# Kernel tuning notes

Measured on AMD Instinct MI355X. Metric: run time of the kernel, lower is better.

## Reference

```python
import jax, jax.numpy as jnp
from jax import lax
import numpy as np

B, C_IN, F, T = 8, 16, 1024, 512
D = 1024          # rnn_hidden_size == rnn_input_size
L = 4             # rnn_num_layers
N_TOKENS = 512
RES_REDUCE = 2


def setup_inputs() -> dict:
    key = jax.random.key(0)
    ks = jax.random.split(key, 8)
    fused_feats = jax.random.normal(ks[0], (B, C_IN, F, T), dtype=jnp.float32)
    s_audio_length = jax.random.randint(ks[1], (B,), 1, T + 1, dtype=jnp.int64)
    # 1x1 conv: C_IN -> 1 channel
    conv_w = jax.random.normal(ks[2], (C_IN,), dtype=jnp.float32) * (1.0 / np.sqrt(C_IN))
    conv_b = jnp.zeros((1,), dtype=jnp.float32)
    # SRU per-layer params (all layers have d_in == D): W [L, D, 3D], v [L, 2D], b [L, 2D]
    sru_W = jax.random.normal(ks[3], (L, D, 3 * D), dtype=jnp.float32) * (1.0 / np.sqrt(D))
    sru_v = jax.random.normal(ks[4], (L, 2 * D), dtype=jnp.float32) * 0.1
    sru_b = jnp.zeros((L, 2 * D), dtype=jnp.float32)
    fc_w = jax.random.normal(ks[5], (D, N_TOKENS), dtype=jnp.float32) * (1.0 / np.sqrt(D))
    fc_b = jnp.zeros((N_TOKENS,), dtype=jnp.float32)
    return dict(fused_feats=fused_feats, s_audio_length=s_audio_length,
                conv_w=conv_w, conv_b=conv_b,
                sru_W=sru_W, sru_v=sru_v, sru_b=sru_b,
                fc_w=fc_w, fc_b=fc_b)


def _sru_layer(x, W, v, b):
    # x: [T, B, D]; W: [D, 3D]; v, b: [2D]
    d = W.shape[1] // 3
    U = jnp.einsum('tbi,ik->tbk', x, W).reshape(x.shape[0], x.shape[1], 3, d)
    x_tilde, f_pre, r_pre = U[..., 0, :], U[..., 1, :], U[..., 2, :]
    vf, vr = v[:d], v[d:]
    bf, br = b[:d], b[d:]

    def step(c, inp):
        xt_t, fp_t = inp
        f = jax.nn.sigmoid(fp_t + vf * c + bf)
        c_new = f * c + (1.0 - f) * xt_t
        return c_new, c_new

    c0 = jnp.zeros((x.shape[1], d), dtype=x.dtype)
    _, cs = lax.scan(step, c0, (x_tilde, f_pre))            # cs: [T, B, D]
    r = jax.nn.sigmoid(r_pre + vr * cs + br)                # reset uses c_t
    return r * cs + (1.0 - r) * x                           # highway residual


def reference(fused_feats, s_audio_length, conv_w, conv_b, sru_W, sru_v, sru_b, fc_w, fc_b):
    # 1x1 conv over channel dim + ReLU: [B, C, F, T] -> [B, F, T]
    x = jax.nn.relu(jnp.einsum('bcft,c->bft', fused_feats, conv_w) + conv_b[0])
    x = x.transpose(2, 0, 1)                                # [T, B, F]
    for l in range(L):
        x = _sru_layer(x, sru_W[l], sru_v[l], sru_b[l])
    rnn_out = x.transpose(1, 0, 2)                          # [B, T, D]
    tokens_logits = jnp.einsum('btd,dk->btk', rnn_out, fc_w) + fc_b
    return tokens_logits, s_audio_length // RES_REDUCE
```

## Files before the change

kernel.cpp:

```cpp
#include <hip/hip_runtime.h>
#include <cstddef>
#include <cstdint>

static constexpr int B_  = 8;
static constexpr int CIN = 16;
static constexpr int F_  = 1024;
static constexpr int T_  = 512;
static constexpr int D_  = 1024;
static constexpr int L_  = 4;
static constexpr int NT  = 512;
static constexpr int M_  = T_ * B_;
static constexpr int K3  = 3 * D_;
static constexpr int NP  = 4 * D_;

typedef __attribute__((ext_vector_type(8))) short short8;
typedef __attribute__((ext_vector_type(4))) float floatx4;

__device__ __forceinline__ unsigned short f2bf(float f) {
    unsigned int u = __builtin_bit_cast(unsigned int, f);
    u += 0x7FFFu + ((u >> 16) & 1u);
    return (unsigned short)(u >> 16);
}
__device__ __forceinline__ float bf2f(unsigned short s) {
    unsigned int u = ((unsigned int)s) << 16;
    return __builtin_bit_cast(float, u);
}

#define GLD16(g, l)                                                              \
    __builtin_amdgcn_global_load_lds(                                            \
        (__attribute__((address_space(1))) unsigned int*)(g),                    \
        (__attribute__((address_space(3))) unsigned int*)(l), 16, 0, 0)

__global__ __launch_bounds__(256) void conv_relu_tr(
    const float* __restrict__ feats, const float* __restrict__ wv,
    const float* __restrict__ bv, unsigned short* __restrict__ x0) {
    __shared__ float tile[32][68];
    const int b  = blockIdx.z;
    const int f0 = blockIdx.y * 32;
    const int t0 = blockIdx.x * 64;
    const float bias = bv[0];

    const int t4 = threadIdx.x & 15;
    const int fi = threadIdx.x >> 4;
    #pragma unroll
    for (int fo = 0; fo < 32; fo += 16) {
        const int f = fo + fi;
        float4 acc = {bias, bias, bias, bias};
        const float* p = feats + (((size_t)b * CIN) * F_ + (f0 + f)) * T_ + t0 + t4 * 4;
        #pragma unroll
        for (int c = 0; c < CIN; ++c) {
            const float4 vv = *(const float4*)(p + (size_t)c * F_ * T_);
            const float w = wv[c];
            acc.x += w * vv.x; acc.y += w * vv.y;
            acc.z += w * vv.z; acc.w += w * vv.w;
        }
        acc.x = fmaxf(acc.x, 0.f); acc.y = fmaxf(acc.y, 0.f);
        acc.z = fmaxf(acc.z, 0.f); acc.w = fmaxf(acc.w, 0.f);
        *(float4*)&tile[f][t4 * 4] = acc;
    }
    __syncthreads();
    const int f4 = threadIdx.x & 7;
    const int tr = threadIdx.x >> 3;
    #pragma unroll
    for (int to = 0; to < 64; to += 32) {
        const int t = to + tr;
        unsigned short pk[4];
        #pragma unroll
        for (int q = 0; q < 4; ++q) pk[q] = f2bf(tile[f4 * 4 + q][t]);
        *(uint2*)&x0[(size_t)(t0 + t) * (B_ * D_) + (size_t)b * D_ + f0 + f4 * 4] =
            *(const uint2*)pk;
    }
}

__global__ __launch_bounds__(256) void prep_weights(
    const float* __restrict__ sru_W, const float* __restrict__ fc_w,
    unsigned short* __restrict__ Wt, unsigned short* __restrict__ WtF) {
    __shared__ float tile[32][33];
    const int z  = blockIdx.z;
    const int x  = threadIdx.x & 31;
    const int y8 = threadIdx.x >> 5;
    if (z < 16) {
        const int l = z >> 2, j = z & 3;
        const int d0 = blockIdx.x * 32;
        const int k0 = blockIdx.y * 32;
        unsigned short* Wo = Wt + (size_t)l * ((size_t)NP * D_);
        if (j < 3) {
            const float* W = sru_W + (size_t)l * D_ * K3;
            #pragma unroll
            for (int yo = 0; yo < 32; yo += 8)
                tile[yo + y8][x] = W[(size_t)(k0 + yo + y8) * K3 + j * D_ + d0 + x];
            __syncthreads();
            #pragma unroll
            for (int yo = 0; yo < 32; yo += 8) {
                const int dy = yo + y8;
                Wo[(size_t)((d0 + dy) * 4 + j) * D_ + k0 + x] = f2bf(tile[x][dy]);
            }
        } else {
            #pragma unroll
            for (int yo = 0; yo < 32; yo += 8) {
                const int dy = d0 + yo + y8;
                Wo[(size_t)(dy * 4 + 3) * D_ + k0 + x] =
                    (k0 + x == dy) ? (unsigned short)0x3F80u : (unsigned short)0u;
            }
        }
    } else {
        if (blockIdx.x >= NT / 32) return;
        const int n0 = blockIdx.x * 32;
        const int k0 = blockIdx.y * 32;
        #pragma unroll
        for (int yo = 0; yo < 32; yo += 8)
            tile[yo + y8][x] = fc_w[(size_t)(k0 + yo + y8) * NT + n0 + x];
        __syncthreads();
        #pragma unroll
        for (int yo = 0; yo < 32; yo += 8)
            WtF[(size_t)(n0 + yo + y8) * D_ + k0 + x] = f2bf(tile[x][yo + y8]);
    }
}

template <int MODE>
__global__ __launch_bounds__(256) void gemm_mfma(
    const unsigned short* __restrict__ A,
    const unsigned short* __restrict__ Bt,
    void* __restrict__ Cv, const float* __restrict__ bias,
    int N, int K) {
    __shared__ unsigned short As[128 * 32];
    __shared__ unsigned short Bs[128 * 32];

    const int tid  = threadIdx.x;
    const int lane = tid & 63;
    const int wid  = tid >> 6;
    const int m0 = blockIdx.y * 128;
    const int n0 = blockIdx.x * 128;
    const int wm = (wid >> 1) * 64;
    const int wn = (wid & 1) * 64;

    floatx4 acc[4][4];
    #pragma unroll
    for (int mi = 0; mi < 4; ++mi)
        #pragma unroll
        for (int ni = 0; ni < 4; ++ni)
            acc[mi][ni] = (floatx4){0.f, 0.f, 0.f, 0.f};

    const char* gA = (const char*)A;
    const char* gB = (const char*)Bt;
    const size_t rowstride = (size_t)K * 2;
    const size_t rA0 = (size_t)(m0 + (tid >> 2)) * rowstride + (tid & 3) * 16;
    const size_t rB0 = (size_t)(n0 + (tid >> 2)) * rowstride + (tid & 3) * 16;
    const size_t pstep = 64 * rowstride;
    char* sA = (char*)As;
    char* sB = (char*)Bs;
    const int ldsbase = wid * 1024;

    const int rsel = lane & 15;
    const int koff = (lane >> 4) * 16;

    for (int k0 = 0; k0 < K; k0 += 32) {
        const size_t kb = (size_t)k0 * 2;
        GLD16(gA + rA0 + kb,         sA + ldsbase);
        GLD16(gA + rA0 + kb + pstep, sA + ldsbase + 4096);
        GLD16(gB + rB0 + kb,         sB + ldsbase);
        GLD16(gB + rB0 + kb + pstep, sB + ldsbase + 4096);
        __syncthreads();

        short8 af[4], bfv[4];
        #pragma unroll
        for (int mi = 0; mi < 4; ++mi)
            af[mi] = *(const short8*)(sA + ((wm + mi * 16 + rsel) * 64 + koff));
        #pragma unroll
        for (int ni = 0; ni < 4; ++ni)
            bfv[ni] = *(const short8*)(sB + ((wn + ni * 16 + rsel) * 64 + koff));
        #pragma unroll
        for (int mi = 0; mi < 4; ++mi)
            #pragma unroll
            for (int ni = 0; ni < 4; ++ni)
                acc[mi][ni] = __builtin_amdgcn_mfma_f32_16x16x32_bf16(
                    af[mi], bfv[ni], acc[mi][ni], 0, 0, 0);
        __syncthreads();
    }

    const int cl = lane & 15;
    const int qr = lane >> 4;
    #pragma unroll
    for (int mi = 0; mi < 4; ++mi) {
        #pragma unroll
        for (int ni = 0; ni < 4; ++ni) {
            const int gn = n0 + wn + ni * 16 + cl;
            #pragma unroll
            for (int i = 0; i < 4; ++i) {
                const int gm = m0 + wm + mi * 16 + qr * 4 + i;
                if (MODE == 0) {
                    ((unsigned short*)Cv)[(size_t)gm * N + gn] = f2bf(acc[mi][ni][i]);
                } else {
                    const int t  = gm >> 3;
                    const int bb = gm & 7;
                    ((float*)Cv)[((size_t)bb * T_ + t) * NT + gn] =
                        acc[mi][ni][i] + bias[gn];
                }
            }
        }
    }
}

__global__ __launch_bounds__(64) void sru_scan(
    const unsigned short* __restrict__ U4,
    const float* __restrict__ v, const float* __restrict__ bvec,
    unsigned short* __restrict__ h) {
    const int idx = blockIdx.x * 64 + threadIdx.x;
    const int d  = idx & (D_ - 1);

    const float vfn = -v[d];
    const float vrn = -v[D_ + d];
    const float bf_ = bvec[d];
    const float br_ = bvec[D_ + d];

    const uint2* up = (const uint2*)U4 + idx;
    unsigned short* hp = h + idx;

    constexpr int UNR  = 8;
    constexpr int PIPE = 4;
    constexpr int NB   = T_ / UNR;
    constexpr size_t ST = (size_t)B_ * D_;

    uint2 ub[PIPE][UNR];
    #pragma unroll
    for (int p = 0; p < PIPE; ++p)
        #pragma unroll
        for (int j = 0; j < UNR; ++j)
            ub[p][j] = up[(size_t)(p * UNR + j) * ST];

    float c = 0.0f;
    for (int bt = 0; bt < NB; bt += PIPE) {
        #pragma unroll
        for (int p = 0; p < PIPE; ++p) {
            const int s = bt + p;
            #pragma unroll
            for (int j = 0; j < UNR; ++j) {
                const uint2 u = ub[p][j];
                const float xt  = bf2f((unsigned short)(u.x & 0xFFFFu));
                const float fpp = bf2f((unsigned short)(u.x >> 16));
                const float rpp = bf2f((unsigned short)(u.y & 0xFFFFu));
                const float xi  = bf2f((unsigned short)(u.y >> 16));
                const float e1 = __expf(fmaf(vfn, c, -(fpp + bf_)));
                const float f  = __builtin_amdgcn_rcpf(1.0f + e1);
                c = fmaf(f, c - xt, xt);
                const float e2 = __expf(fmaf(vrn, c, -(rpp + br_)));
                const float r  = __builtin_amdgcn_rcpf(1.0f + e2);
                hp[(size_t)(s * UNR + j) * ST] = f2bf(fmaf(r, c - xi, xi));
            }
            if (s + PIPE < NB) {
                #pragma unroll
                for (int j = 0; j < UNR; ++j)
                    ub[p][j] = up[(size_t)((s + PIPE) * UNR + j) * ST];
            }
        }
    }
}

__global__ void lens_k(const int* __restrict__ lens, float* __restrict__ out) {
    const int i = threadIdx.x;
    if (i < B_) out[i] = (float)(lens[i] >> 1);
}

extern "C" void kernel_launch(void* const* d_in, const int* in_sizes, int n_in,
                              void* d_out, int out_size, void* d_ws, size_t ws_size,
                              hipStream_t stream) {
    const float* feats  = (const float*)d_in[0];
    const int*   lens   = (const int*)d_in[1];
    const float* conv_w = (const float*)d_in[2];
    const float* conv_b = (const float*)d_in[3];
    const float* sru_W  = (const float*)d_in[4];
    const float* sru_v  = (const float*)d_in[5];
    const float* sru_b  = (const float*)d_in[6];
    const float* fc_w   = (const float*)d_in[7];
    const float* fc_b   = (const float*)d_in[8];
    float* out = (float*)d_out;

    unsigned short* x0 = (unsigned short*)d_ws;
    unsigned short* x1 = x0 + (size_t)M_ * D_;
    unsigned short* U4 = x1 + (size_t)M_ * D_;
    unsigned short* Wt = U4 + (size_t)M_ * NP;
    unsigned short* WtF = Wt + (size_t)L_ * NP * D_;

    conv_relu_tr<<<dim3(T_ / 64, F_ / 32, B_), 256, 0, stream>>>(
        feats, conv_w, conv_b, x0);

    prep_weights<<<dim3(32, 32, 17), 256, 0, stream>>>(sru_W, fc_w, Wt, WtF);

    unsigned short* cur = x0;
    unsigned short* nxt = x1;
    for (int l = 0; l < L_; ++l) {
        gemm_mfma<0><<<dim3(NP / 128, M_ / 128), 256, 0, stream>>>(
            cur, Wt + (size_t)l * NP * D_, U4, nullptr, NP, D_);
        sru_scan<<<(B_ * D_) / 64, 64, 0, stream>>>(
            U4, sru_v + (size_t)l * 2 * D_, sru_b + (size_t)l * 2 * D_, nxt);
        unsigned short* tmp = cur; cur = nxt; nxt = tmp;
    }

    gemm_mfma<1><<<dim3(NT / 128, M_ / 128), 256, 0, stream>>>(
        cur, WtF, out, fc_b, NT, D_);

    lens_k<<<1, 64, 0, stream>>>(lens, out + (size_t)M_ * NT);
}
```

Baseline: 810.0 us.

## Add 256x256 triple-buffered MFMA GEMM for SRU gate projections

```diff
diff --git a/kernel.cpp b/kernel.cpp
--- a/kernel.cpp
+++ b/kernel.cpp
@@ -201,6 +201,129 @@
     }
 }
 
+#define KT_BODY(CB, PB, KT2, DO_STAGE)                                        \
+    {                                                                         \
+        if (DO_STAGE) {                                                       \
+            const size_t gk = (size_t)(KT2) * 64;                             \
+            _Pragma("unroll") for (int s = 0; s < 2; ++s)                     \
+                GLD16(Ab + (size_t)grow[s] * 2048 + gk + gcol[s],             \
+                      (PB) + ((s * 8 + wid) << 10));                          \
+            _Pragma("unroll") for (int s = 0; s < 2; ++s)                     \
+                GLD16(Bb + (size_t)grow[s] * 2048 + gk + gcol[s],             \
+                      (PB) + 16384 + ((s * 8 + wid) << 10));                  \
+        }                                                                     \
+        short8 af[8], bfv[4];                                                 \
+        _Pragma("unroll") for (int mi = 0; mi < 8; ++mi)                      \
+            af[mi] = *(const short8*)((CB) + aoff[mi]);                       \
+        _Pragma("unroll") for (int ni = 0; ni < 4; ++ni)                      \
+            bfv[ni] = *(const short8*)((CB) + boff[ni]);                      \
+        __builtin_amdgcn_s_setprio(1);                                        \
+        _Pragma("unroll") for (int mi = 0; mi < 8; ++mi)                      \
+            _Pragma("unroll") for (int ni = 0; ni < 4; ++ni)                  \
+                acc[mi][ni] = __builtin_amdgcn_mfma_f32_16x16x32_bf16(        \
+                    af[mi], bfv[ni], acc[mi][ni], 0, 0, 0);                   \
+        __builtin_amdgcn_s_setprio(0);                                        \
+    }
+
+__global__ __launch_bounds__(512, 2) void gemm256_gate(
+    const unsigned short* __restrict__ A,
+    const unsigned short* __restrict__ Bt,
+    unsigned short* __restrict__ C) {
+    __shared__ unsigned short lds[49152];
+    char* const sb = (char*)lds;
+
+    const int tid  = threadIdx.x;
+    const int lane = tid & 63;
+    const int wid  = tid >> 6;
+    const int wm   = wid >> 2;
+    const int wn   = wid & 3;
+    const int m0   = blockIdx.y * 256;
+    const int n0   = blockIdx.x * 256;
+
+    const char* Ab = (const char*)A  + (size_t)m0 * 2048;
+    const char* Bb = (const char*)Bt + (size_t)n0 * 2048;
+
+    int grow[2], gcol[2];
+    #pragma unroll
+    for (int s = 0; s < 2; ++s) {
+        const int q  = ((s * 8 + wid) << 10) + lane * 16;
+        const int qs = q ^ (((q >> 7) & 3) << 4);
+        grow[s] = qs >> 6;
+        gcol[s] = qs & 63;
+    }
+    const int rl = lane & 15;
+    const int kb = (lane >> 4) * 16;
+    int aoff[8], boff[4];
+    #pragma unroll
+    for (int mi = 0; mi < 8; ++mi) {
+        const int q = (wm * 128 + mi * 16 + rl) * 64 + kb;
+        aoff[mi] = q ^ (((q >> 7) & 3) << 4);
+    }
+    #pragma unroll
+    for (int ni = 0; ni < 4; ++ni) {
+        const int q = (wn * 64 + ni * 16 + rl) * 64 + kb;
+        boff[ni] = 16384 + (q ^ (((q >> 7) & 3) << 4));
+    }
+
+    floatx4 acc[8][4];
+    #pragma unroll
+    for (int mi = 0; mi < 8; ++mi)
+        #pragma unroll
+        for (int ni = 0; ni < 4; ++ni)
+            acc[mi][ni] = (floatx4){0.f, 0.f, 0.f, 0.f};
+
+    char* const b0 = sb;
+    char* const b1 = sb + 32768;
+    char* const b2 = sb + 65536;
+
+    #pragma unroll
+    for (int t = 0; t < 2; ++t) {
+        char* pb = sb + t * 32768;
+        const size_t gk = (size_t)t * 64;
+        #pragma unroll
+        for (int s = 0; s < 2; ++s)
+            GLD16(Ab + (size_t)grow[s] * 2048 + gk + gcol[s],
+                  pb + ((s * 8 + wid) << 10));
+        #pragma unroll
+        for (int s = 0; s < 2; ++s)
+            GLD16(Bb + (size_t)grow[s] * 2048 + gk + gcol[s],
+                  pb + 16384 + ((s * 8 + wid) << 10));
+    }
+    asm volatile("s_waitcnt vmcnt(4)" ::: "memory");
+    __builtin_amdgcn_s_barrier();
+
+    for (int kt = 0; kt < 30; kt += 3) {
+        KT_BODY(b0, b2, kt + 2, true);
+        asm volatile("s_waitcnt vmcnt(4)" ::: "memory");
+        __builtin_amdgcn_s_barrier();
+        KT_BODY(b1, b0, kt + 3, true);
+        asm volatile("s_waitcnt vmcnt(4)" ::: "memory");
+        __builtin_amdgcn_s_barrier();
+        KT_BODY(b2, b1, kt + 4, true);
+        asm volatile("s_waitcnt vmcnt(4)" ::: "memory");
+        __builtin_amdgcn_s_barrier();
+    }
+    KT_BODY(b0, b2, 0, false);
+    asm volatile("s_waitcnt vmcnt(0)" ::: "memory");
+    __builtin_amdgcn_s_barrier();
+    KT_BODY(b1, b0, 0, false);
+
+    const int cl = lane & 15;
+    const int qr = lane >> 4;
+    #pragma unroll
+    for (int mi = 0; mi < 8; ++mi) {
+        #pragma unroll
+        for (int ni = 0; ni < 4; ++ni) {
+            const int gn = n0 + wn * 64 + ni * 16 + cl;
+            #pragma unroll
+            for (int i = 0; i < 4; ++i) {
+                const int gm = m0 + wm * 128 + mi * 16 + qr * 4 + i;
+                C[(size_t)gm * NP + gn] = f2bf(acc[mi][ni][i]);
+            }
+        }
+    }
+}
+
 __global__ __launch_bounds__(64) void sru_scan(
     const unsigned short* __restrict__ U4,
     const float* __restrict__ v, const float* __restrict__ bvec,
@@ -289,8 +412,8 @@
     unsigned short* cur = x0;
     unsigned short* nxt = x1;
     for (int l = 0; l < L_; ++l) {
-        gemm_mfma<0><<<dim3(NP / 128, M_ / 128), 256, 0, stream>>>(
-            cur, Wt + (size_t)l * NP * D_, U4, nullptr, NP, D_);
+        gemm256_gate<<<dim3(NP / 256, M_ / 256), 512, 0, stream>>>(
+            cur, Wt + (size_t)l * NP * D_, U4);
         sru_scan<<<(B_ * D_) / 64, 64, 0, stream>>>(
             U4, sru_v + (size_t)l * 2 * D_, sru_b + (size_t)l * 2 * D_, nxt);
         unsigned short* tmp = cur; cur = nxt; nxt = tmp;
```

After: 723.5 us. 10.7% less time.
